# Performance work log

Measured on AMD Instinct MI355X. Metric: run time of the kernel, lower is better.

Reference implementation:

```python
import jax, jax.numpy as jnp
import numpy as np

N = 20000   # genes
E = 200000  # global edges
P = 300     # pathways
EP = 2000   # edges per pathway (global node indices)
D = 3       # in_dim == number of omics (forced by nn.Linear(3,1))


def setup_inputs():
    key = jax.random.key(0)
    ks = jax.random.split(key, 20)
    f = lambda i, shape: jax.random.normal(ks[i], shape, dtype=jnp.float32) * 0.1
    return {
        "x": f(0, (N, D)),
        "edge_index": jax.random.randint(ks[1], (2, E), 0, N),
        "path_edges": jax.random.randint(ks[2], (P, 2, EP), 0, N),
        "W_pool": f(3, (D, D)), "b_pool": f(4, (D,)),
        "W_self": f(5, (D, D)), "W_neigh": f(6, (D, D)), "b_conv": f(7, (D,)),
        "sub_Wl": f(8, (P, D, D)), "sub_bl": f(9, (P, D)), "sub_Wr": f(10, (P, D, D)),
        "pool_Wrel": f(11, (P, D, 1)), "pool_Wroot": f(12, (P, D, 1)), "pool_b": f(13, (P, 1)),
        "gate_W": f(14, (P, D, 1)), "gate_b": f(15, (P, 1)),
        "lin_W": f(16, (D, 1)), "lin_b": f(17, (1,)),
        "mlp_W": f(18, (P, 1)), "mlp_b": f(19, (1,)),
    }


def reference(x, edge_index, path_edges, W_pool, b_pool, W_self, W_neigh, b_conv,
              sub_Wl, sub_bl, sub_Wr, pool_Wrel, pool_Wroot, pool_b,
              gate_W, gate_b, lin_W, lin_b, mlp_W, mlp_b):
    n = x.shape[0]
    # add_self_loops on the global edge_index
    loops = jnp.arange(n)
    src = jnp.concatenate([edge_index[0], loops])
    dst = jnp.concatenate([edge_index[1], loops])

    # global SAGEConv with 'pool' aggregator: max_j relu(W_pool h_j), then self + neigh
    hp = jax.nn.relu(x @ W_pool + b_pool)                       # [N,D]
    agg = jax.ops.segment_max(hp[src], dst, num_segments=n)     # [N,D] (self-loops -> no empty segments)
    h = jnp.tanh(x @ W_self + agg @ W_neigh + b_conv)           # [N,D]

    k = int(np.ceil(0.8 * n))  # SAGPooling ratio=0.8 over all N nodes (full x is passed per pathway)

    def per_path(pe, Wl, bl, Wr, Wrel, Wroot, pb, gW, gb):
        s, d = pe[0], pe[1]
        # SAGEConv (mean aggr) on pathway subgraph edges over full node set
        msum = jax.ops.segment_sum(h[s], d, num_segments=n)
        cnt = jax.ops.segment_sum(jnp.ones(s.shape, h.dtype), d, num_segments=n)
        mean = msum / jnp.maximum(cnt, 1.0)[:, None]
        xc = jax.nn.relu(mean @ Wl + bl + h @ Wr)               # [N,D]
        # SAGPooling score via GraphConv (add aggr): W_rel * sum_j x_j + W_root * x + b
        asum = jax.ops.segment_sum(xc[s], d, num_segments=n)
        score = (asum @ Wrel + xc @ Wroot + pb)[:, 0]           # [N]
        topv, perm = jax.lax.top_k(score, k)
        xk = xc[perm] * jnp.tanh(topv)[:, None]                 # [k,D]
        # GlobalAttention readout: softmax gate over kept nodes
        gate = jax.nn.softmax((xk @ gW + gb)[:, 0])             # [k]
        return jax.nn.relu(gate @ xk)                            # [D]

    readout = jax.vmap(per_path)(path_edges, sub_Wl, sub_bl, sub_Wr,
                                 pool_Wrel, pool_Wroot, pool_b, gate_W, gate_b)  # [P,D]
    r = jax.nn.relu(readout @ lin_W + lin_b).T                  # [1,P]
    # mlp: Dropout (identity in eval) -> ReLU -> Linear(P,1) -> Sigmoid
    return jax.nn.sigmoid(jax.nn.relu(r) @ mlp_W + mlp_b)       # [1,1]
```

## Files before the change

kernel.cpp:

```cpp
#include <hip/hip_runtime.h>
#include <math.h>

#define MAXM 2048
#define BMW  640
#define BS   1024
#define NB   2048

__device__ __forceinline__ unsigned fkey(float f){
  unsigned u = __float_as_uint(f);
  return (u & 0x80000000u) ? ~u : (u | 0x80000000u);
}
__device__ __forceinline__ int lbin(float sc, float lo, float scl){
  int b = (int)((sc - lo) * scl);
  return b < 0 ? 0 : (b > NB-1 ? NB-1 : b);
}
__device__ __forceinline__ void hp_eval(const float* __restrict__ x, int i,
                                        const float* __restrict__ Wp,
                                        const float* __restrict__ bp, float* o){
  float x0 = x[i*3+0], x1 = x[i*3+1], x2 = x[i*3+2];
  #pragma unroll
  for (int j = 0; j < 3; ++j)
    o[j] = fmaxf(x0*Wp[0*3+j] + x1*Wp[1*3+j] + x2*Wp[2*3+j] + bp[j], 0.f);
}

__global__ void k_edge(const float* __restrict__ x, const int* __restrict__ ei,
                       const float* __restrict__ Wp, const float* __restrict__ bp,
                       float* __restrict__ agg, float* __restrict__ acc,
                       unsigned* __restrict__ counter, int E){
  if (blockIdx.x == 0 && threadIdx.x == 0){ acc[0] = 0.f; counter[0] = 0u; }
  int e = blockIdx.x*blockDim.x + threadIdx.x;
  if (e >= E) return;
  int s = ei[e], d = ei[E+e];
  float o[3]; hp_eval(x, s, Wp, bp, o);
  #pragma unroll
  for (int j = 0; j < 3; ++j)
    atomicMax((int*)&agg[d*3+j], __float_as_int(o[j]));
}

__global__ void k_h2(const float* __restrict__ x, float* __restrict__ hb,
                     const float* __restrict__ Wp, const float* __restrict__ bp,
                     const float* __restrict__ Ws, const float* __restrict__ Wn,
                     const float* __restrict__ bc, int N){
  int i = blockIdx.x*blockDim.x + threadIdx.x;
  if (i >= N) return;
  float hp[3]; hp_eval(x, i, Wp, bp, hp);
  float x0 = x[i*3+0], x1 = x[i*3+1], x2 = x[i*3+2];
  float a0 = fmaxf(hb[i*3+0], hp[0]);
  float a1 = fmaxf(hb[i*3+1], hp[1]);
  float a2 = fmaxf(hb[i*3+2], hp[2]);
  float o[3];
  #pragma unroll
  for (int j = 0; j < 3; ++j){
    float v = x0*Ws[0*3+j] + x1*Ws[1*3+j] + x2*Ws[2*3+j]
            + a0*Wn[0*3+j] + a1*Wn[1*3+j] + a2*Wn[2*3+j] + bc[j];
    o[j] = tanhf(v);
  }
  hb[i*3+0] = o[0]; hb[i*3+1] = o[1]; hb[i*3+2] = o[2];
}

__device__ __forceinline__ void pick_bucket(const unsigned* hist, int l,
    unsigned pref, unsigned mask, int shift,
    unsigned* sel_prefix, unsigned* sel_mask, int* sel_r){
  unsigned h0 = hist[4*l+0], h1 = hist[4*l+1], h2 = hist[4*l+2], h3 = hist[4*l+3];
  unsigned s = h0+h1+h2+h3;
  unsigned S = s;
  #pragma unroll
  for (int off = 1; off < 64; off <<= 1){
    unsigned t = __shfl_down(S, off);
    if (l + off < 64) S += t;
  }
  unsigned Snext = S - s;
  unsigned r = (unsigned)*sel_r;
  unsigned suf3 = h3 + Snext;
  unsigned suf2 = h2 + suf3;
  unsigned suf1 = h1 + suf2;
  unsigned suf0 = h0 + suf1;
  int b = -1; unsigned sufnext = 0;
  if      (suf3 >= r && Snext < r){ b = 4*l+3; sufnext = Snext; }
  else if (suf2 >= r && suf3  < r){ b = 4*l+2; sufnext = suf3; }
  else if (suf1 >= r && suf2  < r){ b = 4*l+1; sufnext = suf2; }
  else if (suf0 >= r && suf1  < r){ b = 4*l+0; sufnext = suf1; }
  if (b >= 0){
    *sel_prefix = pref | ((unsigned)b << shift);
    *sel_mask   = mask | (255u << shift);
    *sel_r      = (int)(r - sufnext);
  }
}

__global__ void __launch_bounds__(BS)
k_mega(const float* __restrict__ h, const int* __restrict__ pe,
       const float* __restrict__ sWl, const float* __restrict__ sbl, const float* __restrict__ sWr,
       const float* __restrict__ pWrel, const float* __restrict__ pWroot, const float* __restrict__ pB,
       const float* __restrict__ gW, const float* __restrict__ gB,
       const float* __restrict__ linW, const float* __restrict__ linb,
       const float* __restrict__ mlpW, const float* __restrict__ mlpb,
       float* __restrict__ spG, float* __restrict__ acc, unsigned* __restrict__ counter,
       unsigned* __restrict__ out, int N, int EP, int K, int P){
  __shared__ unsigned bm[BMW];
  __shared__ int      wpfx[BMW];
  __shared__ float    msum[MAXM*3];
  __shared__ unsigned scrA[NB];
  __shared__ unsigned scrB[NB];
  __shared__ float    wredf[(BS/64)*4];
  __shared__ float    s_mn, s_mx;
  __shared__ float    rlo[3], rsc[3];
  __shared__ int      rb[3];
  __shared__ int      s_r, s_C, s_cc, s_done;
  __shared__ unsigned s_uT;
  __shared__ unsigned sel_prefix, sel_mask;
  __shared__ int      sel_r;

  const int p = blockIdx.x;
  const int tid = threadIdx.x;

  float Wl[9], Wr[9], bl[3], wrel[3], wroot[3], gw[3];
  #pragma unroll
  for (int j = 0; j < 9; ++j){ Wl[j] = sWl[p*9+j]; Wr[j] = sWr[p*9+j]; }
  #pragma unroll
  for (int j = 0; j < 3; ++j){
    bl[j] = sbl[p*3+j]; wrel[j] = pWrel[p*3+j];
    wroot[j] = pWroot[p*3+j]; gw[j] = gW[p*3+j];
  }
  float pbv = pB[p], gbv = gB[p];
  float* sp = spG + (size_t)p*N;

  int*   cnt  = (int*)scrA;
  float* adot = (float*)scrB;

  for (int s = tid; s < MAXM; s += BS){
    cnt[s] = 0; adot[s] = 0.f;
    msum[s*3+0]=0.f; msum[s*3+1]=0.f; msum[s*3+2]=0.f;
  }
  for (int s = tid; s < BMW; s += BS) bm[s] = 0u;
  if (tid == 0){ s_done = 0; s_uT = 0u; }
  __syncthreads();

  const int* ps = pe + (size_t)p*2*EP;
  const int* pd = ps + EP;

  for (int e = tid; e < EP; e += BS) atomicOr(&bm[pd[e]>>5], 1u << (pd[e]&31));
  __syncthreads();
  if (tid < 64){
    int l = tid, base = l*10;
    int c[10], s = 0;
    #pragma unroll
    for (int q = 0; q < 10; ++q){ c[q] = __popc(bm[base+q]); s += c[q]; }
    int pre = s;
    #pragma unroll
    for (int off = 1; off < 64; off <<= 1){
      int t = __shfl_up(pre, off);
      if (l >= off) pre += t;
    }
    pre -= s;
    #pragma unroll
    for (int q = 0; q < 10; ++q){ wpfx[base+q] = pre; pre += c[q]; }
  }
  __syncthreads();
  for (int e = tid; e < EP; e += BS){
    int s = ps[e], d = pd[e];
    int r = wpfx[d>>5] + __popc(bm[d>>5] & ((1u << (d&31)) - 1u));
    atomicAdd(&cnt[r], 1);
    atomicAdd(&msum[r*3+0], h[s*3+0]);
    atomicAdd(&msum[r*3+1], h[s*3+1]);
    atomicAdd(&msum[r*3+2], h[s*3+2]);
  }
  __syncthreads();
  for (int r = tid; r < MAXM; r += BS){
    int c = cnt[r];
    if (c > 0){
      float inv = 1.f / (float)c;
      msum[r*3+0] *= inv; msum[r*3+1] *= inv; msum[r*3+2] *= inv;
    }
  }
  __syncthreads();
  for (int e = tid; e < EP; e += BS){
    int s = ps[e], d = pd[e];
    float m0=0.f,m1=0.f,m2=0.f;
    unsigned w = bm[s>>5];
    if ((w >> (s&31)) & 1u){
      int rs = wpfx[s>>5] + __popc(w & ((1u << (s&31)) - 1u));
      m0 = msum[rs*3+0]; m1 = msum[rs*3+1]; m2 = msum[rs*3+2];
    }
    float h0 = h[s*3+0], h1 = h[s*3+1], h2 = h[s*3+2];
    float x0 = fmaxf(m0*Wl[0]+m1*Wl[3]+m2*Wl[6] + bl[0] + h0*Wr[0]+h1*Wr[3]+h2*Wr[6], 0.f);
    float x1 = fmaxf(m0*Wl[1]+m1*Wl[4]+m2*Wl[7] + bl[1] + h0*Wr[1]+h1*Wr[4]+h2*Wr[7], 0.f);
    float x2 = fmaxf(m0*Wl[2]+m1*Wl[5]+m2*Wl[8] + bl[2] + h0*Wr[2]+h1*Wr[5]+h2*Wr[8], 0.f);
    int rd = wpfx[d>>5] + __popc(bm[d>>5] & ((1u << (d&31)) - 1u));
    atomicAdd(&adot[rd], x0*wrel[0] + x1*wrel[1] + x2*wrel[2]);
  }
  __syncthreads();

  float mn = 3.0e38f, mx = -3.0e38f;
  for (int i = tid; i < N; i += BS){
    float m0=0.f,m1=0.f,m2=0.f,ad=0.f;
    unsigned w = bm[i>>5];
    if ((w >> (i&31)) & 1u){
      int r = wpfx[i>>5] + __popc(w & ((1u << (i&31)) - 1u));
      m0 = msum[r*3+0]; m1 = msum[r*3+1]; m2 = msum[r*3+2];
      ad = adot[r];
    }
    float h0 = h[i*3+0], h1 = h[i*3+1], h2 = h[i*3+2];
    float x0 = fmaxf(m0*Wl[0]+m1*Wl[3]+m2*Wl[6] + bl[0] + h0*Wr[0]+h1*Wr[3]+h2*Wr[6], 0.f);
    float x1 = fmaxf(m0*Wl[1]+m1*Wl[4]+m2*Wl[7] + bl[1] + h0*Wr[1]+h1*Wr[4]+h2*Wr[7], 0.f);
    float x2 = fmaxf(m0*Wl[2]+m1*Wl[5]+m2*Wl[8] + bl[2] + h0*Wr[2]+h1*Wr[5]+h2*Wr[8], 0.f);
    float sc = ad + x0*wroot[0]+x1*wroot[1]+x2*wroot[2] + pbv;
    sp[i] = sc;
    mn = fminf(mn, sc); mx = fmaxf(mx, sc);
  }
  #pragma unroll
  for (int off = 32; off > 0; off >>= 1){
    mn = fminf(mn, __shfl_down(mn, off));
    mx = fmaxf(mx, __shfl_down(mx, off));
  }
  if ((tid & 63) == 0){ int w = tid>>6; wredf[w*2+0] = mn; wredf[w*2+1] = mx; }
  __syncthreads();
  if (tid == 0){
    float a = 3.0e38f, b = -3.0e38f;
    for (int w = 0; w < BS/64; ++w){ a = fminf(a, wredf[w*2+0]); b = fmaxf(b, wredf[w*2+1]); }
    s_mn = a; s_mx = b; s_r = K;
    if (!(b > a)){ s_uT = fkey(a); s_done = 1; }
  }
  __syncthreads();

  unsigned* hist = scrA;
  unsigned* cand = scrB;

  for (int t = 0; t < 3; ++t){
    __syncthreads();
    if (s_done) break;
    float lo, hi;
    if (t == 0){ lo = s_mn; hi = s_mx; }
    else { lo = rlo[t-1] + rb[t-1]/rsc[t-1]; hi = rlo[t-1] + (rb[t-1]+1)/rsc[t-1]; }
    float scl = 2047.0f / (hi - lo);
    if (!(hi > lo) || !(scl < 1e37f)){
      if (tid == 0){ s_uT = fkey(lo); s_done = 1; }
      __syncthreads();
      continue;
    }
    for (int b = tid; b < NB; b += BS) hist[b] = 0u;
    __syncthreads();
    if (t == 0){
      if ((N & 3) == 0){
        int G = N >> 2;
        for (int g = tid; g < G; g += BS){
          float4 v = ((const float4*)sp)[g];
          atomicAdd(&hist[lbin(v.x, lo, scl)], 1u);
          atomicAdd(&hist[lbin(v.y, lo, scl)], 1u);
          atomicAdd(&hist[lbin(v.z, lo, scl)], 1u);
          atomicAdd(&hist[lbin(v.w, lo, scl)], 1u);
        }
      } else {
        for (int i = tid; i < N; i += BS) atomicAdd(&hist[lbin(sp[i], lo, scl)], 1u);
      }
    } else {
      for (int i = tid; i < N; i += BS){
        float sc = sp[i];
        bool act = true;
        for (int q = 0; q < t; ++q) act = act && (lbin(sc, rlo[q], rsc[q]) == rb[q]);
        if (act) atomicAdd(&hist[lbin(sc, lo, scl)], 1u);
      }
    }
    __syncthreads();
    if (tid < 64){
      int l = tid;
      unsigned s = 0;
      for (int q = 0; q < 32; ++q) s += hist[l*32+q];
      unsigned S = s;
      #pragma unroll
      for (int off = 1; off < 64; off <<= 1){
        unsigned u2 = __shfl_down(S, off);
        if (l + off < 64) S += u2;
      }
      unsigned suf = S - s;
      unsigned r = (unsigned)s_r;
      int b = -1; unsigned sufnext = 0, cb = 0;
      for (int q = 31; q >= 0; --q){
        unsigned c = hist[l*32+q];
        unsigned nsuf = suf + c;
        if (nsuf >= r && suf < r){ b = l*32+q; sufnext = suf; cb = c; }
        suf = nsuf;
      }
      if (b >= 0){
        rb[t] = b; rlo[t] = lo; rsc[t] = scl;
        s_r = (int)(r - sufnext);
        s_C = (int)cb;
      }
    }
    __syncthreads();
    int C = s_C;
    if (C <= NB){
      if (tid == 0) s_cc = 0;
      __syncthreads();
      for (int i = tid; i < N; i += BS){
        float sc = sp[i];
        bool act = true;
        for (int q = 0; q <= t; ++q) act = act && (lbin(sc, rlo[q], rsc[q]) == rb[q]);
        if (act){ int ix = atomicAdd(&s_cc, 1); if (ix < NB) cand[ix] = fkey(sc); }
      }
      __syncthreads();
      if (tid == 0){ sel_prefix = 0u; sel_mask = 0u; sel_r = s_r; }
      __syncthreads();
      for (int pass = 0; pass < 4; ++pass){
        int shift = 24 - 8*pass;
        if (tid < 256) hist[tid] = 0u;
        __syncthreads();
        unsigned mask = sel_mask, pref = sel_prefix;
        for (int j = tid; j < C; j += BS){
          unsigned u = cand[j];
          if ((u & mask) == pref) atomicAdd(&hist[(u>>shift)&255u], 1u);
        }
        __syncthreads();
        if (tid < 64)
          pick_bucket(hist, tid, pref, mask, shift, &sel_prefix, &sel_mask, &sel_r);
        __syncthreads();
      }
      if (tid == 0){ s_uT = sel_prefix; s_done = 1; }
      __syncthreads();
    } else if (t == 2){
      if (tid == 0){ s_uT = fkey(lo + rb[t]/scl); s_done = 1; }
      __syncthreads();
    }
  }
  __syncthreads();
  const unsigned uT = s_uT;

  float l = 0.f, a0 = 0.f, a1 = 0.f, a2 = 0.f;
  for (int i = tid; i < N; i += BS){
    float sc = sp[i];
    if (fkey(sc) >= uT){
      float m0=0.f,m1=0.f,m2=0.f;
      unsigned w = bm[i>>5];
      if ((w >> (i&31)) & 1u){
        int r = wpfx[i>>5] + __popc(w & ((1u << (i&31)) - 1u));
        m0 = msum[r*3+0]; m1 = msum[r*3+1]; m2 = msum[r*3+2];
      }
      float h0 = h[i*3+0], h1 = h[i*3+1], h2 = h[i*3+2];
      float x0 = fmaxf(m0*Wl[0]+m1*Wl[3]+m2*Wl[6] + bl[0] + h0*Wr[0]+h1*Wr[3]+h2*Wr[6], 0.f);
      float x1 = fmaxf(m0*Wl[1]+m1*Wl[4]+m2*Wl[7] + bl[1] + h0*Wr[1]+h1*Wr[4]+h2*Wr[7], 0.f);
      float x2 = fmaxf(m0*Wl[2]+m1*Wl[5]+m2*Wl[8] + bl[2] + h0*Wr[2]+h1*Wr[5]+h2*Wr[8], 0.f);
      float tt = tanhf(sc);
      x0 *= tt; x1 *= tt; x2 *= tt;
      float g = x0*gw[0] + x1*gw[1] + x2*gw[2] + gbv;
      g = fminf(fmaxf(g, -60.f), 60.f);
      float e = expf(g);
      l += e; a0 += e*x0; a1 += e*x1; a2 += e*x2;
    }
  }
  #pragma unroll
  for (int off = 32; off > 0; off >>= 1){
    l  += __shfl_down(l,  off);
    a0 += __shfl_down(a0, off);
    a1 += __shfl_down(a1, off);
    a2 += __shfl_down(a2, off);
  }
  if ((tid & 63) == 0){
    int w = tid >> 6;
    wredf[w*4+0]=l; wredf[w*4+1]=a0; wredf[w*4+2]=a1; wredf[w*4+3]=a2;
  }
  __syncthreads();
  if (tid == 0){
    float L=0.f, A0=0.f, A1=0.f, A2=0.f;
    for (int w = 0; w < BS/64; ++w){
      L += wredf[w*4+0]; A0 += wredf[w*4+1]; A1 += wredf[w*4+2]; A2 += wredf[w*4+3];
    }
    float inv = 1.f / L;
    float r0 = fmaxf(A0*inv, 0.f);
    float r1 = fmaxf(A1*inv, 0.f);
    float r2 = fmaxf(A2*inv, 0.f);
    float rr = fmaxf(r0*linW[0] + r1*linW[1] + r2*linW[2] + linb[0], 0.f);
    atomicAdd(acc, rr * mlpW[p]);
    __threadfence();
    unsigned old = atomicAdd(counter, 1u);
    if (old == (unsigned)(P-1)){
      __threadfence();
      float z = atomicAdd(acc, 0.f) + mlpb[0];
      float a = 1.f / (1.f + expf(-z));
      unsigned A = __float_as_uint(a);
      unsigned B = (A + 0x7FFFu + ((A >> 16) & 1u)) >> 16;
      out[0] = (A & 0xFFFF0000u) | (B & 0xFFFFu);
    }
  }
}

extern "C" void kernel_launch(void* const* d_in, const int* in_sizes, int n_in,
                              void* d_out, int out_size, void* d_ws, size_t ws_size,
                              hipStream_t stream){
  const float* x      = (const float*)d_in[0];
  const int*   ei     = (const int*)  d_in[1];
  const int*   pe     = (const int*)  d_in[2];
  const float* W_pool = (const float*)d_in[3];
  const float* b_pool = (const float*)d_in[4];
  const float* W_self = (const float*)d_in[5];
  const float* W_neigh= (const float*)d_in[6];
  const float* b_conv = (const float*)d_in[7];
  const float* sWl    = (const float*)d_in[8];
  const float* sbl    = (const float*)d_in[9];
  const float* sWr    = (const float*)d_in[10];
  const float* pWrel  = (const float*)d_in[11];
  const float* pWroot = (const float*)d_in[12];
  const float* pB     = (const float*)d_in[13];
  const float* gW     = (const float*)d_in[14];
  const float* gB     = (const float*)d_in[15];
  const float* linW   = (const float*)d_in[16];
  const float* linb   = (const float*)d_in[17];
  const float* mlpW   = (const float*)d_in[18];
  const float* mlpb   = (const float*)d_in[19];

  const int N  = in_sizes[0] / 3;
  const int E  = in_sizes[1] / 2;
  const int P  = in_sizes[13];
  const int EP = in_sizes[2] / (2 * P);
  const int K  = (4*N + 4) / 5;

  float*    ws      = (float*)d_ws;
  float*    acc     = ws;
  unsigned* counter = (unsigned*)(ws + 1);
  float*    agg     = ws + 16;
  float*    h       = agg;
  float*    spG     = ws + 16 + (size_t)3*N;

  k_edge<<<(E+255)/256, 256, 0, stream>>>(x, ei, W_pool, b_pool, agg, acc, counter, E);
  k_h2  <<<(N+255)/256, 256, 0, stream>>>(x, agg, W_pool, b_pool,
                                          W_self, W_neigh, b_conv, N);
  k_mega<<<P, BS, 0, stream>>>(h, pe, sWl, sbl, sWr, pWrel, pWroot, pB, gW, gB,
                               linW, linb, mlpW, mlpb,
                               spG, acc, counter, (unsigned*)d_out, N, EP, K, P);
}
```

Baseline: 252.6 us.

## Fuse top-k histogram into score pass and compute readout as total minus excluded

```diff
diff --git a/kernel.cpp b/kernel.cpp
--- a/kernel.cpp
+++ b/kernel.cpp
@@ -4,15 +4,11 @@
 #define MAXM 2048
 #define BMW  640
 #define BS   1024
-#define NB   2048
+#define NBC  2048
 
 __device__ __forceinline__ unsigned fkey(float f){
   unsigned u = __float_as_uint(f);
   return (u & 0x80000000u) ? ~u : (u | 0x80000000u);
-}
-__device__ __forceinline__ int lbin(float sc, float lo, float scl){
-  int b = (int)((sc - lo) * scl);
-  return b < 0 ? 0 : (b > NB-1 ? NB-1 : b);
 }
 __device__ __forceinline__ void hp_eval(const float* __restrict__ x, int i,
                                         const float* __restrict__ Wp,
@@ -34,7 +30,8 @@
   float o[3]; hp_eval(x, s, Wp, bp, o);
   #pragma unroll
   for (int j = 0; j < 3; ++j)
-    atomicMax((int*)&agg[d*3+j], __float_as_int(o[j]));
+    if (o[j] > 0.f)
+      atomicMax((int*)&agg[d*3+j], __float_as_int(o[j]));
 }
 
 __global__ void k_h2(const float* __restrict__ x, float* __restrict__ hb,
@@ -58,32 +55,30 @@
   hb[i*3+0] = o[0]; hb[i*3+1] = o[1]; hb[i*3+2] = o[2];
 }
 
-__device__ __forceinline__ void pick_bucket(const unsigned* hist, int l,
-    unsigned pref, unsigned mask, int shift,
-    unsigned* sel_prefix, unsigned* sel_mask, int* sel_r){
-  unsigned h0 = hist[4*l+0], h1 = hist[4*l+1], h2 = hist[4*l+2], h3 = hist[4*l+3];
-  unsigned s = h0+h1+h2+h3;
+__device__ __forceinline__ void pick2(const unsigned* hist, int l, int shift,
+    unsigned* sel_prefix, unsigned* sel_mask, int* sel_r, int* sel_C){
+  unsigned hq[4];
+  hq[0]=hist[4*l+0]; hq[1]=hist[4*l+1]; hq[2]=hist[4*l+2]; hq[3]=hist[4*l+3];
+  unsigned s = hq[0]+hq[1]+hq[2]+hq[3];
   unsigned S = s;
   #pragma unroll
   for (int off = 1; off < 64; off <<= 1){
     unsigned t = __shfl_down(S, off);
     if (l + off < 64) S += t;
   }
-  unsigned Snext = S - s;
+  unsigned suf = S - s;
   unsigned r = (unsigned)*sel_r;
-  unsigned suf3 = h3 + Snext;
-  unsigned suf2 = h2 + suf3;
-  unsigned suf1 = h1 + suf2;
-  unsigned suf0 = h0 + suf1;
-  int b = -1; unsigned sufnext = 0;
-  if      (suf3 >= r && Snext < r){ b = 4*l+3; sufnext = Snext; }
-  else if (suf2 >= r && suf3  < r){ b = 4*l+2; sufnext = suf3; }
-  else if (suf1 >= r && suf2  < r){ b = 4*l+1; sufnext = suf2; }
-  else if (suf0 >= r && suf1  < r){ b = 4*l+0; sufnext = suf1; }
+  int b = -1; unsigned sufnext = 0, cb = 0;
+  for (int q = 3; q >= 0; --q){
+    unsigned c = hq[q], nsuf = suf + c;
+    if (nsuf >= r && suf < r){ b = 4*l+q; sufnext = suf; cb = c; }
+    suf = nsuf;
+  }
   if (b >= 0){
-    *sel_prefix = pref | ((unsigned)b << shift);
-    *sel_mask   = mask | (255u << shift);
-    *sel_r      = (int)(r - sufnext);
+    *sel_prefix |= (unsigned)b << shift;
+    *sel_mask   |= 255u << shift;
+    *sel_r       = (int)(r - sufnext);
+    *sel_C       = (int)cb;
   }
 }
 
@@ -99,14 +94,11 @@
   __shared__ unsigned bm[BMW];
   __shared__ int      wpfx[BMW];
   __shared__ float    msum[MAXM*3];
-  __shared__ unsigned scrA[NB];
-  __shared__ unsigned scrB[NB];
-  __shared__ float    wredf[(BS/64)*4];
-  __shared__ float    s_mn, s_mx;
-  __shared__ float    rlo[3], rsc[3];
-  __shared__ int      rb[3];
-  __shared__ int      s_r, s_C, s_cc, s_done;
-  __shared__ unsigned s_uT;
+  __shared__ unsigned scrA[4096];
+  __shared__ unsigned scrB[NBC];
+  __shared__ float    wredA[(BS/64)*4];
+  __shared__ float    wredB[(BS/64)*4];
+  __shared__ int      s_C, s_cc;
   __shared__ unsigned sel_prefix, sel_mask;
   __shared__ int      sel_r;
 
@@ -127,12 +119,13 @@
   int*   cnt  = (int*)scrA;
   float* adot = (float*)scrB;
 
+  for (int s = tid; s < 4096; s += BS) scrA[s] = 0u;
   for (int s = tid; s < MAXM; s += BS){
-    cnt[s] = 0; adot[s] = 0.f;
+    adot[s] = 0.f;
     msum[s*3+0]=0.f; msum[s*3+1]=0.f; msum[s*3+2]=0.f;
   }
   for (int s = tid; s < BMW; s += BS) bm[s] = 0u;
-  if (tid == 0){ s_done = 0; s_uT = 0u; }
+  if (tid == 0){ sel_r = K; sel_prefix = 0u; sel_mask = 0u; s_C = 0; }
   __syncthreads();
 
   const int* ps = pe + (size_t)p*2*EP;
@@ -167,6 +160,7 @@
   __syncthreads();
   for (int r = tid; r < MAXM; r += BS){
     int c = cnt[r];
+    cnt[r] = 0;
     if (c > 0){
       float inv = 1.f / (float)c;
       msum[r*3+0] *= inv; msum[r*3+1] *= inv; msum[r*3+2] *= inv;
@@ -190,7 +184,7 @@
   }
   __syncthreads();
 
-  float mn = 3.0e38f, mx = -3.0e38f;
+  float tl = 0.f, ta0 = 0.f, ta1 = 0.f, ta2 = 0.f;
   for (int i = tid; i < N; i += BS){
     float m0=0.f,m1=0.f,m2=0.f,ad=0.f;
     unsigned w = bm[i>>5];
@@ -205,129 +199,103 @@
     float x2 = fmaxf(m0*Wl[2]+m1*Wl[5]+m2*Wl[8] + bl[2] + h0*Wr[2]+h1*Wr[5]+h2*Wr[8], 0.f);
     float sc = ad + x0*wroot[0]+x1*wroot[1]+x2*wroot[2] + pbv;
     sp[i] = sc;
-    mn = fminf(mn, sc); mx = fmaxf(mx, sc);
+    unsigned u = fkey(sc);
+    atomicAdd(&scrA[u >> 20], 1u << (((u >> 19) & 1u) << 4));
+    float tt = tanhf(sc);
+    float g = fminf(fmaxf(tt*(x0*gw[0]+x1*gw[1]+x2*gw[2]) + gbv, -60.f), 60.f);
+    float e = expf(g);
+    float et = e * tt;
+    tl += e; ta0 += et*x0; ta1 += et*x1; ta2 += et*x2;
   }
   #pragma unroll
   for (int off = 32; off > 0; off >>= 1){
-    mn = fminf(mn, __shfl_down(mn, off));
-    mx = fmaxf(mx, __shfl_down(mx, off));
-  }
-  if ((tid & 63) == 0){ int w = tid>>6; wredf[w*2+0] = mn; wredf[w*2+1] = mx; }
-  __syncthreads();
-  if (tid == 0){
-    float a = 3.0e38f, b = -3.0e38f;
-    for (int w = 0; w < BS/64; ++w){ a = fminf(a, wredf[w*2+0]); b = fmaxf(b, wredf[w*2+1]); }
-    s_mn = a; s_mx = b; s_r = K;
-    if (!(b > a)){ s_uT = fkey(a); s_done = 1; }
-  }
-  __syncthreads();
-
-  unsigned* hist = scrA;
-  unsigned* cand = scrB;
-
-  for (int t = 0; t < 3; ++t){
-    __syncthreads();
-    if (s_done) break;
-    float lo, hi;
-    if (t == 0){ lo = s_mn; hi = s_mx; }
-    else { lo = rlo[t-1] + rb[t-1]/rsc[t-1]; hi = rlo[t-1] + (rb[t-1]+1)/rsc[t-1]; }
-    float scl = 2047.0f / (hi - lo);
-    if (!(hi > lo) || !(scl < 1e37f)){
-      if (tid == 0){ s_uT = fkey(lo); s_done = 1; }
+    tl  += __shfl_down(tl,  off); ta0 += __shfl_down(ta0, off);
+    ta1 += __shfl_down(ta1, off); ta2 += __shfl_down(ta2, off);
+  }
+  if ((tid & 63) == 0){
+    int w = tid >> 6;
+    wredA[w*4+0]=tl; wredA[w*4+1]=ta0; wredA[w*4+2]=ta1; wredA[w*4+3]=ta2;
+  }
+  __syncthreads();
+
+  if (tid < 64){
+    int l = tid;
+    const unsigned* hw = scrA + l*64;
+    unsigned s = 0;
+    for (int q = 0; q < 64; ++q){ unsigned w = hw[q]; s += (w & 0xFFFFu) + (w >> 16); }
+    unsigned S = s;
+    #pragma unroll
+    for (int off = 1; off < 64; off <<= 1){
+      unsigned t = __shfl_down(S, off);
+      if (l + off < 64) S += t;
+    }
+    unsigned suf = S - s;
+    unsigned r = (unsigned)sel_r;
+    int b = -1; unsigned sufnext = 0, cb = 0;
+    for (int q = 127; q >= 0; --q){
+      unsigned w = hw[q>>1];
+      unsigned c = (q & 1) ? (w >> 16) : (w & 0xFFFFu);
+      unsigned nsuf = suf + c;
+      if (nsuf >= r && suf < r){ b = l*128 + q; sufnext = suf; cb = c; }
+      suf = nsuf;
+    }
+    if (b >= 0){
+      sel_prefix = (unsigned)b << 19;
+      sel_mask   = 0xFFF80000u;
+      sel_r      = (int)(r - sufnext);
+      s_C        = (int)cb;
+    }
+  }
+
+  const int SHIFTS[3] = {11, 3, 0};
+  int lvl = 0;
+  while (true){
+    __syncthreads();
+    if (s_C <= NBC || lvl >= 3 || sel_mask == 0xFFFFFFFFu) break;
+    int sh = SHIFTS[lvl];
+    if (tid < 256) scrA[tid] = 0u;
+    __syncthreads();
+    unsigned mk = sel_mask, pf = sel_prefix;
+    for (int i = tid; i < N; i += BS){
+      unsigned u = fkey(sp[i]);
+      if ((u & mk) == pf) atomicAdd(&scrA[(u >> sh) & 255u], 1u);
+    }
+    __syncthreads();
+    if (tid < 64) pick2(scrA, tid, sh, &sel_prefix, &sel_mask, &sel_r, &s_C);
+    lvl++;
+  }
+
+  if (sel_mask != 0xFFFFFFFFu){
+    if (tid == 0) s_cc = 0;
+    __syncthreads();
+    unsigned mk = sel_mask, pf = sel_prefix;
+    for (int i = tid; i < N; i += BS){
+      unsigned u = fkey(sp[i]);
+      if ((u & mk) == pf){ int ix = atomicAdd(&s_cc, 1); if (ix < NBC) scrB[ix] = u; }
+    }
+    __syncthreads();
+    int C = s_cc < NBC ? s_cc : NBC;
+    for (int q = lvl; q < 3; ++q){
+      int sh = SHIFTS[q];
+      if (tid < 256) scrA[tid] = 0u;
       __syncthreads();
-      continue;
-    }
-    for (int b = tid; b < NB; b += BS) hist[b] = 0u;
-    __syncthreads();
-    if (t == 0){
-      if ((N & 3) == 0){
-        int G = N >> 2;
-        for (int g = tid; g < G; g += BS){
-          float4 v = ((const float4*)sp)[g];
-          atomicAdd(&hist[lbin(v.x, lo, scl)], 1u);
-          atomicAdd(&hist[lbin(v.y, lo, scl)], 1u);
-          atomicAdd(&hist[lbin(v.z, lo, scl)], 1u);
-          atomicAdd(&hist[lbin(v.w, lo, scl)], 1u);
-        }
-      } else {
-        for (int i = tid; i < N; i += BS) atomicAdd(&hist[lbin(sp[i], lo, scl)], 1u);
-      }
-    } else {
-      for (int i = tid; i < N; i += BS){
-        float sc = sp[i];
-        bool act = true;
-        for (int q = 0; q < t; ++q) act = act && (lbin(sc, rlo[q], rsc[q]) == rb[q]);
-        if (act) atomicAdd(&hist[lbin(sc, lo, scl)], 1u);
-      }
-    }
-    __syncthreads();
-    if (tid < 64){
-      int l = tid;
-      unsigned s = 0;
-      for (int q = 0; q < 32; ++q) s += hist[l*32+q];
-      unsigned S = s;
-      #pragma unroll
-      for (int off = 1; off < 64; off <<= 1){
-        unsigned u2 = __shfl_down(S, off);
-        if (l + off < 64) S += u2;
-      }
-      unsigned suf = S - s;
-      unsigned r = (unsigned)s_r;
-      int b = -1; unsigned sufnext = 0, cb = 0;
-      for (int q = 31; q >= 0; --q){
-        unsigned c = hist[l*32+q];
-        unsigned nsuf = suf + c;
-        if (nsuf >= r && suf < r){ b = l*32+q; sufnext = suf; cb = c; }
-        suf = nsuf;
-      }
-      if (b >= 0){
-        rb[t] = b; rlo[t] = lo; rsc[t] = scl;
-        s_r = (int)(r - sufnext);
-        s_C = (int)cb;
-      }
-    }
-    __syncthreads();
-    int C = s_C;
-    if (C <= NB){
-      if (tid == 0) s_cc = 0;
-      __syncthreads();
-      for (int i = tid; i < N; i += BS){
-        float sc = sp[i];
-        bool act = true;
-        for (int q = 0; q <= t; ++q) act = act && (lbin(sc, rlo[q], rsc[q]) == rb[q]);
-        if (act){ int ix = atomicAdd(&s_cc, 1); if (ix < NB) cand[ix] = fkey(sc); }
+      unsigned mk2 = sel_mask, pf2 = sel_prefix;
+      for (int j = tid; j < C; j += BS){
+        unsigned u = scrB[j];
+        if ((u & mk2) == pf2) atomicAdd(&scrA[(u >> sh) & 255u], 1u);
       }
       __syncthreads();
-      if (tid == 0){ sel_prefix = 0u; sel_mask = 0u; sel_r = s_r; }
+      if (tid < 64) pick2(scrA, tid, sh, &sel_prefix, &sel_mask, &sel_r, &s_C);
       __syncthreads();
-      for (int pass = 0; pass < 4; ++pass){
-        int shift = 24 - 8*pass;
-        if (tid < 256) hist[tid] = 0u;
-        __syncthreads();
-        unsigned mask = sel_mask, pref = sel_prefix;
-        for (int j = tid; j < C; j += BS){
-          unsigned u = cand[j];
-          if ((u & mask) == pref) atomicAdd(&hist[(u>>shift)&255u], 1u);
-        }
-        __syncthreads();
-        if (tid < 64)
-          pick_bucket(hist, tid, pref, mask, shift, &sel_prefix, &sel_mask, &sel_r);
-        __syncthreads();
-      }
-      if (tid == 0){ s_uT = sel_prefix; s_done = 1; }
-      __syncthreads();
-    } else if (t == 2){
-      if (tid == 0){ s_uT = fkey(lo + rb[t]/scl); s_done = 1; }
-      __syncthreads();
-    }
-  }
-  __syncthreads();
-  const unsigned uT = s_uT;
-
-  float l = 0.f, a0 = 0.f, a1 = 0.f, a2 = 0.f;
+    }
+  }
+  __syncthreads();
+  const unsigned uT = sel_prefix;
+
+  float dl = 0.f, d0 = 0.f, d1 = 0.f, d2 = 0.f;
   for (int i = tid; i < N; i += BS){
     float sc = sp[i];
-    if (fkey(sc) >= uT){
+    if (fkey(sc) < uT){
       float m0=0.f,m1=0.f,m2=0.f;
       unsigned w = bm[i>>5];
       if ((w >> (i&31)) & 1u){
@@ -339,29 +307,29 @@
       float x1 = fmaxf(m0*Wl[1]+m1*Wl[4]+m2*Wl[7] + bl[1] + h0*Wr[1]+h1*Wr[4]+h2*Wr[7], 0.f);
       float x2 = fmaxf(m0*Wl[2]+m1*Wl[5]+m2*Wl[8] + bl[2] + h0*Wr[2]+h1*Wr[5]+h2*Wr[8], 0.f);
       float tt = tanhf(sc);
-      x0 *= tt; x1 *= tt; x2 *= tt;
-      float g = x0*gw[0] + x1*gw[1] + x2*gw[2] + gbv;
-      g = fminf(fmaxf(g, -60.f), 60.f);
+      float g = fminf(fmaxf(tt*(x0*gw[0]+x1*gw[1]+x2*gw[2]) + gbv, -60.f), 60.f);
       float e = expf(g);
-      l += e; a0 += e*x0; a1 += e*x1; a2 += e*x2;
+      float et = e * tt;
+      dl += e; d0 += et*x0; d1 += et*x1; d2 += et*x2;
     }
   }
   #pragma unroll
   for (int off = 32; off > 0; off >>= 1){
-    l  += __shfl_down(l,  off);
-    a0 += __shfl_down(a0, off);
-    a1 += __shfl_down(a1, off);
-    a2 += __shfl_down(a2, off);
+    dl += __shfl_down(dl, off); d0 += __shfl_down(d0, off);
+    d1 += __shfl_down(d1, off); d2 += __shfl_down(d2, off);
   }
   if ((tid & 63) == 0){
     int w = tid >> 6;
-    wredf[w*4+0]=l; wredf[w*4+1]=a0; wredf[w*4+2]=a1; wredf[w*4+3]=a2;
+    wredB[w*4+0]=dl; wredB[w*4+1]=d0; wredB[w*4+2]=d1; wredB[w*4+3]=d2;
   }
   __syncthreads();
   if (tid == 0){
     float L=0.f, A0=0.f, A1=0.f, A2=0.f;
     for (int w = 0; w < BS/64; ++w){
-      L += wredf[w*4+0]; A0 += wredf[w*4+1]; A1 += wredf[w*4+2]; A2 += wredf[w*4+3];
+      L  += wredA[w*4+0] - wredB[w*4+0];
+      A0 += wredA[w*4+1] - wredB[w*4+1];
+      A1 += wredA[w*4+2] - wredB[w*4+2];
+      A2 += wredA[w*4+3] - wredB[w*4+3];
     }
     float inv = 1.f / L;
     float r0 = fmaxf(A0*inv, 0.f);
```

New measurement: 281.6 us. 11.5% more time.

## Accumulate softmax over all nodes early and subtract the dropped bottom set

Applied to the files above, without the earlier changes.

```diff
diff --git a/kernel.cpp b/kernel.cpp
--- a/kernel.cpp
+++ b/kernel.cpp
@@ -34,7 +34,8 @@
   float o[3]; hp_eval(x, s, Wp, bp, o);
   #pragma unroll
   for (int j = 0; j < 3; ++j)
-    atomicMax((int*)&agg[d*3+j], __float_as_int(o[j]));
+    if (o[j] > 0.f)
+      atomicMax((int*)&agg[d*3+j], __float_as_int(o[j]));
 }
 
 __global__ void k_h2(const float* __restrict__ x, float* __restrict__ hb,
@@ -101,7 +102,9 @@
   __shared__ float    msum[MAXM*3];
   __shared__ unsigned scrA[NB];
   __shared__ unsigned scrB[NB];
-  __shared__ float    wredf[(BS/64)*4];
+  __shared__ float    wredf[(BS/64)*2];
+  __shared__ float    wredA[(BS/64)*4];
+  __shared__ float    wredB[(BS/64)*4];
   __shared__ float    s_mn, s_mx;
   __shared__ float    rlo[3], rsc[3];
   __shared__ int      rb[3];
@@ -191,6 +194,7 @@
   __syncthreads();
 
   float mn = 3.0e38f, mx = -3.0e38f;
+  float tl = 0.f, ta0 = 0.f, ta1 = 0.f, ta2 = 0.f;
   for (int i = tid; i < N; i += BS){
     float m0=0.f,m1=0.f,m2=0.f,ad=0.f;
     unsigned w = bm[i>>5];
@@ -206,13 +210,24 @@
     float sc = ad + x0*wroot[0]+x1*wroot[1]+x2*wroot[2] + pbv;
     sp[i] = sc;
     mn = fminf(mn, sc); mx = fmaxf(mx, sc);
+    float tt = tanhf(sc);
+    float g = fminf(fmaxf(tt*(x0*gw[0]+x1*gw[1]+x2*gw[2]) + gbv, -60.f), 60.f);
+    float e = expf(g);
+    float et = e * tt;
+    tl += e; ta0 += et*x0; ta1 += et*x1; ta2 += et*x2;
   }
   #pragma unroll
   for (int off = 32; off > 0; off >>= 1){
-    mn = fminf(mn, __shfl_down(mn, off));
-    mx = fmaxf(mx, __shfl_down(mx, off));
-  }
-  if ((tid & 63) == 0){ int w = tid>>6; wredf[w*2+0] = mn; wredf[w*2+1] = mx; }
+    mn  = fminf(mn, __shfl_down(mn, off));
+    mx  = fmaxf(mx, __shfl_down(mx, off));
+    tl  += __shfl_down(tl,  off); ta0 += __shfl_down(ta0, off);
+    ta1 += __shfl_down(ta1, off); ta2 += __shfl_down(ta2, off);
+  }
+  if ((tid & 63) == 0){
+    int w = tid >> 6;
+    wredf[w*2+0] = mn; wredf[w*2+1] = mx;
+    wredA[w*4+0]=tl; wredA[w*4+1]=ta0; wredA[w*4+2]=ta1; wredA[w*4+3]=ta2;
+  }
   __syncthreads();
   if (tid == 0){
     float a = 3.0e38f, b = -3.0e38f;
@@ -324,10 +339,10 @@
   __syncthreads();
   const unsigned uT = s_uT;
 
-  float l = 0.f, a0 = 0.f, a1 = 0.f, a2 = 0.f;
+  float dl = 0.f, d0 = 0.f, d1 = 0.f, d2 = 0.f;
   for (int i = tid; i < N; i += BS){
     float sc = sp[i];
-    if (fkey(sc) >= uT){
+    if (fkey(sc) < uT){
       float m0=0.f,m1=0.f,m2=0.f;
       unsigned w = bm[i>>5];
       if ((w >> (i&31)) & 1u){
@@ -339,29 +354,29 @@
       float x1 = fmaxf(m0*Wl[1]+m1*Wl[4]+m2*Wl[7] + bl[1] + h0*Wr[1]+h1*Wr[4]+h2*Wr[7], 0.f);
       float x2 = fmaxf(m0*Wl[2]+m1*Wl[5]+m2*Wl[8] + bl[2] + h0*Wr[2]+h1*Wr[5]+h2*Wr[8], 0.f);
       float tt = tanhf(sc);
-      x0 *= tt; x1 *= tt; x2 *= tt;
-      float g = x0*gw[0] + x1*gw[1] + x2*gw[2] + gbv;
-      g = fminf(fmaxf(g, -60.f), 60.f);
+      float g = fminf(fmaxf(tt*(x0*gw[0]+x1*gw[1]+x2*gw[2]) + gbv, -60.f), 60.f);
       float e = expf(g);
-      l += e; a0 += e*x0; a1 += e*x1; a2 += e*x2;
+      float et = e * tt;
+      dl += e; d0 += et*x0; d1 += et*x1; d2 += et*x2;
     }
   }
   #pragma unroll
   for (int off = 32; off > 0; off >>= 1){
-    l  += __shfl_down(l,  off);
-    a0 += __shfl_down(a0, off);
-    a1 += __shfl_down(a1, off);
-    a2 += __shfl_down(a2, off);
+    dl += __shfl_down(dl, off); d0 += __shfl_down(d0, off);
+    d1 += __shfl_down(d1, off); d2 += __shfl_down(d2, off);
   }
   if ((tid & 63) == 0){
     int w = tid >> 6;
-    wredf[w*4+0]=l; wredf[w*4+1]=a0; wredf[w*4+2]=a1; wredf[w*4+3]=a2;
+    wredB[w*4+0]=dl; wredB[w*4+1]=d0; wredB[w*4+2]=d1; wredB[w*4+3]=d2;
   }
   __syncthreads();
   if (tid == 0){
     float L=0.f, A0=0.f, A1=0.f, A2=0.f;
     for (int w = 0; w < BS/64; ++w){
-      L += wredf[w*4+0]; A0 += wredf[w*4+1]; A1 += wredf[w*4+2]; A2 += wredf[w*4+3];
+      L  += wredA[w*4+0] - wredB[w*4+0];
+      A0 += wredA[w*4+1] - wredB[w*4+1];
+      A1 += wredA[w*4+2] - wredB[w*4+2];
+      A2 += wredA[w*4+3] - wredB[w*4+3];
     }
     float inv = 1.f / L;
     float r0 = fmaxf(A0*inv, 0.f);
```

After: 244.3 us. -3.3%, faster.
